# Kernel optimization log

Measured on AMD Instinct MI355X. Metric: run time of the kernel, lower is better.

Reference implementation:

```python
import jax, jax.numpy as jnp
import numpy as np

BS, SEQ, D, H, NK = 4, 256, 256, 8, 16


def _ln(x, g, b, eps=1e-5):
    m = x.mean(-1, keepdims=True)
    v = ((x - m) ** 2).mean(-1, keepdims=True)
    return (x - m) / jnp.sqrt(v + eps) * g + b


def _attention(q, k, v, mask, gammas, maxout):
    # q,k,v: [b,h,s,dk]; mask: [1,1,s,s] bool; gammas: [h,1,1]
    dk = q.shape[-1]
    scores = jnp.einsum('bhqd,bhkd->bhqk', q, k) / jnp.sqrt(jnp.asarray(dk, q.dtype))
    seqlen = scores.shape[-1]
    ar = jnp.arange(seqlen)
    pos = jnp.abs(ar[None, :] - ar[:, None]).astype(scores.dtype)[None, None]
    # distance-decay term (computed under no_grad in the original)
    s_ = jax.nn.softmax(jnp.where(mask, scores, -1e32), axis=-1)
    distcum = jnp.cumsum(s_, axis=-1)
    disttotal = jnp.sum(s_, axis=-1, keepdims=True)
    dist = jax.lax.stop_gradient(jnp.sqrt(jnp.clip((disttotal - distcum) * pos, 0.0, None)))
    g = -jnp.abs(gammas)[None]  # [1,h,1,1]
    effect = jnp.clip(jnp.exp(dist * g), 1e-5, 1e5)
    scores = scores * effect
    scores = jax.nn.softmax(jnp.where(mask, scores, -1e32), axis=-1)
    scores = jnp.where(mask, scores, 0.0)
    if maxout:
        scale = jnp.minimum(1.0 / (jnp.max(scores, axis=-1, keepdims=True) + 1e-8), 5.0)
        scores = scores * scale
    return jnp.einsum('bhqk,bhkd->bhqd', scores, v), scores


def _mha(xq, xk, xv, Wq, bq, Wk, bk, Wv, bv, Wo, bo, gammas, mask, maxout):
    bs, seq, d = xq.shape
    h = gammas.shape[0]
    dk = d // h
    def heads(x, W, b):
        return (x @ W + b).reshape(bs, seq, h, dk).transpose(0, 2, 1, 3)
    o, sc = _attention(heads(xq, Wq, bq), heads(xk, Wk, bk), heads(xv, Wv, bv), mask, gammas, maxout)
    o = o.transpose(0, 2, 1, 3).reshape(bs, seq, d)
    return o @ Wo + bo, sc


def _block(xq, xk, xv, Wq, bq, Wk, bk, Wv, bv, Wo, bo, gammas, lng, lnb, peek_cur):
    seq = xq.shape[1]
    mask = jnp.tril(jnp.ones((seq, seq), bool), 0 if peek_cur else -1)[None, None]
    out, sc = _mha(xq, xk, xv, Wq, bq, Wk, bk, Wv, bv, Wo, bo, gammas, mask, not peek_cur)
    return _ln(xq + out, lng, lnb), sc


def _dtransformer(q_emb, s_emb, know_params,
                  Wq1, bq1, Wv1, bv1, Wo1, bo1, gam1, lng1, lnb1,
                  Wq2, bq2, Wv2, bv2, Wo2, bo2, gam2, lng2, lnb2,
                  Wq3, bq3, Wv3, bv3, Wo3, bo3, gam3, lng3, lnb3,
                  Wq4, bq4, Wk4, bk4, Wv4, bv4, Wo4, bo4, gam4, lng4, lnb4):
    # n_blocks == 3 path; kq_same=True for blocks 1-3 (Wk := Wq)
    hq, _ = _block(q_emb, q_emb, q_emb, Wq1, bq1, Wq1, bq1, Wv1, bv1, Wo1, bo1, gam1, lng1, lnb1, True)
    hs, _ = _block(s_emb, s_emb, s_emb, Wq2, bq2, Wq2, bq2, Wv2, bv2, Wo2, bo2, gam2, lng2, lnb2, True)
    p, q_scores = _block(hq, hq, hs, Wq3, bq3, Wq3, bq3, Wv3, bv3, Wo3, bo3, gam3, lng3, lnb3, True)
    bs, seq, d = p.shape
    nk = know_params.shape[0]
    query = jnp.broadcast_to(know_params[None, :, None, :], (bs, nk, seq, d)).reshape(bs * nk, seq, d)
    hq_r = jnp.broadcast_to(hq[:, None], (bs, nk, seq, d)).reshape(bs * nk, seq, d)
    p_r = jnp.broadcast_to(p[:, None], (bs, nk, seq, d)).reshape(bs * nk, seq, d)
    z, k_sc = _block(query, hq_r, p_r, Wq4, bq4, Wk4, bk4, Wv4, bv4, Wo4, bo4, gam4, lng4, lnb4, False)
    z = z.reshape(bs, nk, seq, d).transpose(0, 2, 1, 3).reshape(bs, seq, nk * d)
    h = gam4.shape[0]
    k_scores = k_sc.reshape(bs, nk, h, seq, seq).transpose(0, 2, 3, 1, 4)
    return z, q_scores, k_scores


_PARAM_NAMES = []
for _b in ('1', '2', '3', '4'):
    _PARAM_NAMES += ['Wq' + _b, 'bq' + _b]
    if _b == '4':
        _PARAM_NAMES += ['Wk4', 'bk4']
    _PARAM_NAMES += ['Wv' + _b, 'bv' + _b, 'Wo' + _b, 'bo' + _b, 'gam' + _b, 'lng' + _b, 'lnb' + _b]


def setup_inputs() -> dict:
    key = jax.random.key(0)
    ks = jax.random.split(key, 64)
    inp = {}
    inp['q_emb'] = jax.random.normal(ks[0], (BS, SEQ, D), jnp.float32)
    inp['s_emb'] = jax.random.normal(ks[1], (BS, SEQ, D), jnp.float32)
    inp['lens'] = jax.random.randint(ks[2], (BS,), 1, SEQ)
    inp['know_params'] = jax.random.uniform(ks[3], (NK, D), jnp.float32, -1.0, 1.0)
    i = 4
    for name in _PARAM_NAMES:
        if name.startswith('W'):
            inp[name] = jax.random.normal(ks[i], (D, D), jnp.float32) * 0.02; i += 1
        elif name.startswith('b'):
            inp[name] = jnp.zeros((D,), jnp.float32)
        elif name.startswith('gam'):
            inp[name] = jax.random.normal(ks[i], (H, 1, 1), jnp.float32) * 0.3; i += 1
        elif name.startswith('lng'):
            inp[name] = jnp.ones((D,), jnp.float32)
        else:
            inp[name] = jnp.zeros((D,), jnp.float32)
    return inp


def reference(q_emb, s_emb, lens, know_params,
              Wq1, bq1, Wv1, bv1, Wo1, bo1, gam1, lng1, lnb1,
              Wq2, bq2, Wv2, bv2, Wo2, bo2, gam2, lng2, lnb2,
              Wq3, bq3, Wv3, bv3, Wo3, bo3, gam3, lng3, lnb3,
              Wq4, bq4, Wk4, bk4, Wv4, bv4, Wo4, bo4, gam4, lng4, lnb4):
    return _dtransformer(q_emb, s_emb, know_params,
                         Wq1, bq1, Wv1, bv1, Wo1, bo1, gam1, lng1, lnb1,
                         Wq2, bq2, Wv2, bv2, Wo2, bo2, gam2, lng2, lnb2,
                         Wq3, bq3, Wv3, bv3, Wo3, bo3, gam3, lng3, lnb3,
                         Wq4, bq4, Wk4, bk4, Wv4, bv4, Wo4, bo4, gam4, lng4, lnb4)
```

## Files before the change

kernel.cpp:

```cpp
#include <hip/hip_runtime.h>
#include <math.h>

#define SEQL 256
#define DM   256
#define NH   8
#define DKH  32
#define BSZ  4
#define NKN  16

__device__ __forceinline__ float wave_red_sum(float v) {
#pragma unroll
  for (int o = 32; o > 0; o >>= 1) v += __shfl_xor(v, o);
  return v;
}
__device__ __forceinline__ float wave_red_max(float v) {
#pragma unroll
  for (int o = 32; o > 0; o >>= 1) v = fmaxf(v, __shfl_xor(v, o));
  return v;
}
__device__ __forceinline__ float wave_incl_scan(float v) {
  const int lane = threadIdx.x & 63;
#pragma unroll
  for (int o = 1; o < 64; o <<= 1) {
    float u = __shfl_up(v, o);
    if (lane >= o) v += u;
  }
  return v;
}

struct GemmSet { const float* A; const float* W; const float* bias; float* C; int M; };
struct Gemm4 { GemmSet s[4]; };

__global__ __launch_bounds__(256) void dt_gemmN(Gemm4 args) {
  const GemmSet g = args.s[blockIdx.z];
  const int bm = blockIdx.x * 64, bn = blockIdx.y * 64;
  if (bm >= g.M) return;
  __shared__ float As[16][68];
  __shared__ float Bs[16][68];
  const int tid = threadIdx.x;
  const int tc = tid & 15, tr = tid >> 4;
  float acc[4][4] = {};
  for (int k0 = 0; k0 < DM; k0 += 16) {
    {
      const int m = tid >> 2, kq = tid & 3;
      int row = bm + m; row = row < g.M ? row : (g.M - 1);
      const float4 v = *reinterpret_cast<const float4*>(&g.A[(size_t)row * DM + k0 + kq * 4]);
      As[kq * 4 + 0][m] = v.x; As[kq * 4 + 1][m] = v.y;
      As[kq * 4 + 2][m] = v.z; As[kq * 4 + 3][m] = v.w;
    }
    {
      const int k = tid >> 4, nq = tid & 15;
      const float4 v = *reinterpret_cast<const float4*>(&g.W[(size_t)(k0 + k) * DM + bn + nq * 4]);
      *reinterpret_cast<float4*>(&Bs[k][nq * 4]) = v;
    }
    __syncthreads();
#pragma unroll
    for (int k = 0; k < 16; ++k) {
      float a[4], b[4];
#pragma unroll
      for (int i = 0; i < 4; ++i) a[i] = As[k][tr * 4 + i];
#pragma unroll
      for (int j = 0; j < 4; ++j) b[j] = Bs[k][tc * 4 + j];
#pragma unroll
      for (int i = 0; i < 4; ++i)
#pragma unroll
        for (int j = 0; j < 4; ++j) acc[i][j] = fmaf(a[i], b[j], acc[i][j]);
    }
    __syncthreads();
  }
#pragma unroll
  for (int i = 0; i < 4; ++i) {
    const int row = bm + tr * 4 + i;
    if (row >= g.M) continue;
    float4 o;
    o.x = acc[i][0] + g.bias[bn + tc * 4 + 0];
    o.y = acc[i][1] + g.bias[bn + tc * 4 + 1];
    o.z = acc[i][2] + g.bias[bn + tc * 4 + 2];
    o.w = acc[i][3] + g.bias[bn + tc * 4 + 3];
    *reinterpret_cast<float4*>(&g.C[(size_t)row * DM + bn + tc * 4]) = o;
  }
}

__global__ __launch_bounds__(256) void dt_scores_nt2(const float* __restrict__ Q0,
                                                     const float* __restrict__ Q1,
                                                     float* __restrict__ Sa,
                                                     float* __restrict__ Sb) {
  const int z = blockIdx.z;
  const int set = z >> 5, bh = z & 31;
  const float* Qp = set ? Q1 : Q0;
  float* S = set ? Sb : Sa;
  const int b = bh >> 3, h = bh & 7;
  const float* Q = Qp + (size_t)b * SEQL * DM + h * DKH;
  __shared__ float Qs[16][33], Ks[16][33];
  const int tid = threadIdx.x;
  const int tj = tid & 15, ti = tid >> 4;
  const int i0 = blockIdx.x * 16, j0 = blockIdx.y * 16;
  const int r = tid >> 5, c = tid & 31;
  Qs[r][c]     = Q[(size_t)(i0 + r) * DM + c];
  Qs[r + 8][c] = Q[(size_t)(i0 + 8 + r) * DM + c];
  Ks[r][c]     = Q[(size_t)(j0 + r) * DM + c];
  Ks[r + 8][c] = Q[(size_t)(j0 + 8 + r) * DM + c];
  __syncthreads();
  float acc = 0.f;
#pragma unroll
  for (int k = 0; k < DKH; ++k) acc = fmaf(Qs[ti][k], Ks[tj][k], acc);
  S[((size_t)bh * SEQL + i0 + ti) * SEQL + j0 + tj] = acc * 0.17677669529663687f;
}

__global__ __launch_bounds__(256) void dt_scores4(const float* __restrict__ Q4h,
                                                  const float* __restrict__ Kp,
                                                  float* __restrict__ S0) {
  const int idx = blockIdx.x * 256 + threadIdx.x;
  const int j = idx & 255;
  const int h = (idx >> 8) & 7;
  const int nk = (idx >> 11) & 15;
  const int b = idx >> 15;
  const float* q = Q4h + nk * DM + h * DKH;
  const float* k = Kp + ((size_t)(b * SEQL + j)) * DM + h * DKH;
  float acc = 0.f;
#pragma unroll
  for (int c = 0; c < DKH; ++c) acc = fmaf(q[c], k[c], acc);
  S0[idx] = acc * 0.17677669529663687f;
}

__global__ __launch_bounds__(256) void dt_prep4(const float* __restrict__ S0,
                                                float* __restrict__ Pfx) {
  const int wid = threadIdx.x >> 6, lane = threadIdx.x & 63;
  const int row = blockIdx.x * 4 + wid;
  const float4 s4 = *reinterpret_cast<const float4*>(S0 + (size_t)row * SEQL + lane * 4);
  float s[4] = {s4.x, s4.y, s4.z, s4.w};
  float mx = fmaxf(fmaxf(s[0], s[1]), fmaxf(s[2], s[3]));
  mx = wave_red_max(mx);
  float e[4], t = 0.f;
#pragma unroll
  for (int q = 0; q < 4; ++q) { e[q] = __expf(s[q] - mx); t += e[q]; }
  const float incl = wave_incl_scan(t);
  float run = incl - t;
  float4 o;
  run += e[0]; o.x = run;
  run += e[1]; o.y = run;
  run += e[2]; o.z = run;
  run += e[3]; o.w = run;
  *reinterpret_cast<float4*>(Pfx + (size_t)row * SEQL + lane * 4) = o;
}

__global__ __launch_bounds__(256) void dt_softmax13w2(const float* __restrict__ Sa,
                                                      const float* __restrict__ Sb,
                                                      float* __restrict__ Pa,
                                                      float* __restrict__ Pb,
                                                      const float* __restrict__ g0,
                                                      const float* __restrict__ g1) {
  const int wid = threadIdx.x >> 6, lane = threadIdx.x & 63;
  const int grow = blockIdx.x * 4 + wid;
  const int set = grow >> 13;
  const int row = grow & 8191;
  const float* S = set ? Sb : Sa;
  float* P = set ? Pb : Pa;
  const float* gam = set ? g1 : g0;
  const int i = row & 255, h = (row >> 8) & 7;
  const float g = -fabsf(gam[h]);
  const int jb = lane * 4;
  const float4 s4 = *reinterpret_cast<const float4*>(S + (size_t)row * SEQL + jb);
  float s[4] = {s4.x, s4.y, s4.z, s4.w};
  float mx = -1e30f;
#pragma unroll
  for (int q = 0; q < 4; ++q) if (jb + q <= i) mx = fmaxf(mx, s[q]);
  mx = wave_red_max(mx);
  float e[4], t = 0.f;
#pragma unroll
  for (int q = 0; q < 4; ++q) { e[q] = (jb + q <= i) ? __expf(s[q] - mx) : 0.f; t += e[q]; }
  const float incl = wave_incl_scan(t);
  const float total = __shfl(incl, 63);
  const float inv = 1.f / total;
  float run = incl - t;
  float p2[4], t2 = 0.f;
#pragma unroll
  for (int q = 0; q < 4; ++q) {
    run += e[q];
    const float cum = run * inv;
    float dd = (1.f - cum) * (float)(i - jb - q);
    dd = dd > 0.f ? dd : 0.f;
    float eff = __expf(g * sqrtf(dd));
    eff = fmaxf(eff, 1e-5f);
    const float y = s[q] * eff;
    p2[q] = (jb + q <= i) ? __expf(y) : 0.f;
    t2 += p2[q];
  }
  const float sum2 = wave_red_sum(t2);
  const float inv2 = 1.f / sum2;
  float4 o = {p2[0] * inv2, p2[1] * inv2, p2[2] * inv2, p2[3] * inv2};
  *reinterpret_cast<float4*>(P + (size_t)row * SEQL + jb) = o;
}

__global__ __launch_bounds__(256) void dt_sm_pv4(const float* __restrict__ S0,
                                                 const float* __restrict__ Pfx,
                                                 const float* __restrict__ Vp,
                                                 const float* __restrict__ gam,
                                                 float* __restrict__ KS,
                                                 float* __restrict__ O) {
  __shared__ float Vs[256][32];
  __shared__ float Pl[32][260];
  __shared__ float Pfl[256];
  const int z = blockIdx.x;
  const int h = z & 7, b = z >> 7;
  const int nk = (z >> 3) & 15, bnk = z >> 3;
  const int tid = threadIdx.x, lane = tid & 63, w = tid >> 6;
  const float* Vbase = Vp + (size_t)b * SEQL * DM + h * DKH;
  {
    const int j = tid >> 3, c4 = (tid & 7) * 4;
    for (int jj = 0; jj < 256; jj += 32) {
      const float4 v = *reinterpret_cast<const float4*>(Vbase + (size_t)(jj + j) * DM + c4);
      *reinterpret_cast<float4*>(&Vs[jj + j][c4]) = v;
    }
  }
  if (tid < 64) {
    const float4 p = *reinterpret_cast<const float4*>(Pfx + (size_t)z * SEQL + tid * 4);
    *reinterpret_cast<float4*>(&Pfl[tid * 4]) = p;
  }
  const float4 s4 = *reinterpret_cast<const float4*>(S0 + (size_t)z * SEQL + lane * 4);
  const float4 p4 = *reinterpret_cast<const float4*>(Pfx + (size_t)z * SEQL + lane * 4);
  const float s[4] = {s4.x, s4.y, s4.z, s4.w};
  const float pj[4] = {p4.x, p4.y, p4.z, p4.w};
  const float g = -fabsf(gam[h]);
  const int jb = lane * 4;
  __syncthreads();

  for (int chunk = 0; chunk < 8; ++chunk) {
    const int i0 = chunk * 32;
#pragma unroll
    for (int r = 0; r < 8; ++r) {
      const int il = w * 8 + r;
      const int i = i0 + il;
      float pv[4];
      if (i == 0) {
        pv[0] = pv[1] = pv[2] = pv[3] = 0.f;
      } else {
        const float rinv = 1.f / Pfl[i - 1];
        float t = 0.f, m = 0.f;
#pragma unroll
        for (int q = 0; q < 4; ++q) {
          const float cum = pj[q] * rinv;
          float dd = (1.f - cum) * (float)(i - jb - q);
          dd = dd > 0.f ? dd : 0.f;
          float eff = __expf(g * sqrtf(dd));
          eff = fmaxf(eff, 1e-5f);
          const float y = s[q] * eff;
          pv[q] = (jb + q < i) ? __expf(y) : 0.f;
          t += pv[q];
          m = fmaxf(m, pv[q]);
        }
#pragma unroll
        for (int o = 32; o > 0; o >>= 1) {
          t += __shfl_xor(t, o);
          m = fmaxf(m, __shfl_xor(m, o));
        }
        const float inv2 = 1.f / t;
        const float scale = fminf(1.f / (m * inv2 + 1e-8f), 5.f);
        const float f = inv2 * scale;
        pv[0] *= f; pv[1] *= f; pv[2] *= f; pv[3] *= f;
      }
      const float4 o4 = {pv[0], pv[1], pv[2], pv[3]};
      *reinterpret_cast<float4*>(KS + ((((size_t)(b * NH + h)) * SEQL + i) * NKN + nk) * SEQL + jb) = o4;
      *reinterpret_cast<float4*>(&Pl[il][jb]) = o4;
    }
    __syncthreads();
    const int il = tid >> 3, cg = tid & 7;
    float ax = 0.f, ay = 0.f, az = 0.f, aw = 0.f;
#pragma unroll 8
    for (int j4 = 0; j4 < 64; ++j4) {
      const float4 pp = *reinterpret_cast<const float4*>(&Pl[il][j4 * 4]);
      const float4 v0 = *reinterpret_cast<const float4*>(&Vs[j4 * 4 + 0][cg * 4]);
      const float4 v1 = *reinterpret_cast<const float4*>(&Vs[j4 * 4 + 1][cg * 4]);
      const float4 v2 = *reinterpret_cast<const float4*>(&Vs[j4 * 4 + 2][cg * 4]);
      const float4 v3 = *reinterpret_cast<const float4*>(&Vs[j4 * 4 + 3][cg * 4]);
      ax = fmaf(pp.x, v0.x, ax); ax = fmaf(pp.y, v1.x, ax); ax = fmaf(pp.z, v2.x, ax); ax = fmaf(pp.w, v3.x, ax);
      ay = fmaf(pp.x, v0.y, ay); ay = fmaf(pp.y, v1.y, ay); ay = fmaf(pp.z, v2.y, ay); ay = fmaf(pp.w, v3.y, ay);
      az = fmaf(pp.x, v0.z, az); az = fmaf(pp.y, v1.z, az); az = fmaf(pp.z, v2.z, az); az = fmaf(pp.w, v3.z, az);
      aw = fmaf(pp.x, v0.w, aw); aw = fmaf(pp.y, v1.w, aw); aw = fmaf(pp.z, v2.w, aw); aw = fmaf(pp.w, v3.w, aw);
    }
    const float4 oo = {ax, ay, az, aw};
    *reinterpret_cast<float4*>(O + ((size_t)(bnk * SEQL + i0 + il)) * DM + h * DKH + cg * 4) = oo;
    __syncthreads();
  }
}

__global__ __launch_bounds__(256) void dt_pv13_2(const float* __restrict__ Pa,
                                                 const float* __restrict__ Pb,
                                                 const float* __restrict__ V0,
                                                 const float* __restrict__ V1,
                                                 float* __restrict__ Oa,
                                                 float* __restrict__ Ob) {
  __shared__ float Ps[32][33];
  __shared__ float Vs[32][33];
  const int z = blockIdx.y;
  const int set = z >> 5, bh = z & 31;
  const float* P = set ? Pb : Pa;
  const float* Vp = set ? V1 : V0;
  float* O = set ? Ob : Oa;
  const int b = bh >> 3, h = bh & 7;
  const int i0 = blockIdx.x * 32;
  const int tid = threadIdx.x;
  const int c = tid & 31, ir = tid >> 5;
  float acc[4] = {0.f, 0.f, 0.f, 0.f};
  const float* Prow = P + ((size_t)bh * SEQL + i0) * SEQL;
  const float* Vbase = Vp + (size_t)b * SEQL * DM + h * DKH;
  for (int j0 = 0; j0 < SEQL; j0 += 32) {
#pragma unroll
    for (int k = 0; k < 4; ++k) {
      Ps[ir + k * 8][c] = Prow[(size_t)(ir + k * 8) * SEQL + j0 + c];
      Vs[ir + k * 8][c] = Vbase[(size_t)(j0 + ir + k * 8) * DM + c];
    }
    __syncthreads();
#pragma unroll
    for (int jj = 0; jj < 32; ++jj) {
      const float v = Vs[jj][c];
#pragma unroll
      for (int k = 0; k < 4; ++k) acc[k] = fmaf(Ps[ir + k * 8][jj], v, acc[k]);
    }
    __syncthreads();
  }
#pragma unroll
  for (int k = 0; k < 4; ++k)
    O[((size_t)(b * SEQL + i0 + ir + k * 8)) * DM + h * DKH + c] = acc[k];
}

__global__ __launch_bounds__(256) void dt_ln_res2(const float* __restrict__ X0,
                                                  const float* __restrict__ X1,
                                                  const float* __restrict__ Y0,
                                                  const float* __restrict__ Y1,
                                                  const float* __restrict__ G0,
                                                  const float* __restrict__ G1,
                                                  const float* __restrict__ B0,
                                                  const float* __restrict__ B1,
                                                  float* __restrict__ Z0,
                                                  float* __restrict__ Z1) {
  const int wid = threadIdx.x >> 6, lane = threadIdx.x & 63;
  const int grow = blockIdx.x * 4 + wid;
  const int set = grow >> 10;
  const int row = grow & 1023;
  const float* X = set ? X1 : X0;
  const float* Y = set ? Y1 : Y0;
  const float* g = set ? G1 : G0;
  const float* bb = set ? B1 : B0;
  float* Z = set ? Z1 : Z0;
  const int jb = lane * 4;
  const float4 x4 = *reinterpret_cast<const float4*>(X + (size_t)row * DM + jb);
  const float4 y4 = *reinterpret_cast<const float4*>(Y + (size_t)row * DM + jb);
  float x[4] = {x4.x + y4.x, x4.y + y4.y, x4.z + y4.z, x4.w + y4.w};
  const float mean = wave_red_sum(x[0] + x[1] + x[2] + x[3]) * (1.f / 256.f);
  float vs = 0.f;
#pragma unroll
  for (int q = 0; q < 4; ++q) { const float d = x[q] - mean; vs += d * d; }
  const float var = wave_red_sum(vs) * (1.f / 256.f);
  const float rstd = 1.f / sqrtf(var + 1e-5f);
  const float4 g4 = *reinterpret_cast<const float4*>(g + jb);
  const float4 b4 = *reinterpret_cast<const float4*>(bb + jb);
  float4 o;
  o.x = (x[0] - mean) * rstd * g4.x + b4.x;
  o.y = (x[1] - mean) * rstd * g4.y + b4.y;
  o.z = (x[2] - mean) * rstd * g4.z + b4.z;
  o.w = (x[3] - mean) * rstd * g4.w + b4.w;
  *reinterpret_cast<float4*>(Z + (size_t)row * DM + jb) = o;
}

__global__ __launch_bounds__(256) void dt_ln4w(const float* __restrict__ know,
                                               const float* __restrict__ Y,
                                               const float* __restrict__ g,
                                               const float* __restrict__ bb,
                                               float* __restrict__ Z) {
  const int wid = threadIdx.x >> 6, lane = threadIdx.x & 63;
  const int row = blockIdx.x * 4 + wid;
  const int i = row & 255;
  const int nk = (row >> 8) & 15;
  const int b = row >> 12;
  const int jb = lane * 4;
  const float4 k4 = *reinterpret_cast<const float4*>(know + (size_t)nk * DM + jb);
  const float4 y4 = *reinterpret_cast<const float4*>(Y + (size_t)row * DM + jb);
  float x[4] = {k4.x + y4.x, k4.y + y4.y, k4.z + y4.z, k4.w + y4.w};
  const float mean = wave_red_sum(x[0] + x[1] + x[2] + x[3]) * (1.f / 256.f);
  float vs = 0.f;
#pragma unroll
  for (int q = 0; q < 4; ++q) { const float d = x[q] - mean; vs += d * d; }
  const float var = wave_red_sum(vs) * (1.f / 256.f);
  const float rstd = 1.f / sqrtf(var + 1e-5f);
  const float4 g4 = *reinterpret_cast<const float4*>(g + jb);
  const float4 b4 = *reinterpret_cast<const float4*>(bb + jb);
  float4 o;
  o.x = (x[0] - mean) * rstd * g4.x + b4.x;
  o.y = (x[1] - mean) * rstd * g4.y + b4.y;
  o.z = (x[2] - mean) * rstd * g4.z + b4.z;
  o.w = (x[3] - mean) * rstd * g4.w + b4.w;
  *reinterpret_cast<float4*>(Z + ((size_t)(b * SEQL + i)) * (NKN * DM) + (size_t)nk * DM + jb) = o;
}

extern "C" void kernel_launch(void* const* d_in, const int* in_sizes, int n_in,
                              void* d_out, int out_size, void* d_ws, size_t ws_size,
                              hipStream_t stream) {
  (void)in_sizes; (void)n_in; (void)out_size; (void)ws_size;
  const float* q_emb = (const float*)d_in[0];
  const float* s_emb = (const float*)d_in[1];
  const float* know  = (const float*)d_in[3];
  const float* Wq1 = (const float*)d_in[4],  *bq1 = (const float*)d_in[5];
  const float* Wv1 = (const float*)d_in[6],  *bv1 = (const float*)d_in[7];
  const float* Wo1 = (const float*)d_in[8],  *bo1 = (const float*)d_in[9];
  const float* gam1 = (const float*)d_in[10], *lng1 = (const float*)d_in[11], *lnb1 = (const float*)d_in[12];
  const float* Wq2 = (const float*)d_in[13], *bq2 = (const float*)d_in[14];
  const float* Wv2 = (const float*)d_in[15], *bv2 = (const float*)d_in[16];
  const float* Wo2 = (const float*)d_in[17], *bo2 = (const float*)d_in[18];
  const float* gam2 = (const float*)d_in[19], *lng2 = (const float*)d_in[20], *lnb2 = (const float*)d_in[21];
  const float* Wq3 = (const float*)d_in[22], *bq3 = (const float*)d_in[23];
  const float* Wv3 = (const float*)d_in[24], *bv3 = (const float*)d_in[25];
  const float* Wo3 = (const float*)d_in[26], *bo3 = (const float*)d_in[27];
  const float* gam3 = (const float*)d_in[28], *lng3 = (const float*)d_in[29], *lnb3 = (const float*)d_in[30];
  const float* Wq4 = (const float*)d_in[31], *bq4 = (const float*)d_in[32];
  const float* Wk4 = (const float*)d_in[33], *bk4 = (const float*)d_in[34];
  const float* Wv4 = (const float*)d_in[35], *bv4 = (const float*)d_in[36];
  const float* Wo4 = (const float*)d_in[37], *bo4 = (const float*)d_in[38];
  const float* gam4 = (const float*)d_in[39], *lng4 = (const float*)d_in[40], *lnb4 = (const float*)d_in[41];

  float* ws = (float*)d_ws;
  const size_t U = 262144;
  float* Qp0 = ws + 0 * U;
  float* Qp1 = ws + 1 * U;
  float* Vp0 = ws + 2 * U;
  float* Vp1 = ws + 3 * U;
  float* Sa  = ws + 4 * U;
  float* Sb  = ws + 12 * U;
  float* O0  = ws + 20 * U;
  float* O1  = ws + 21 * U;
  float* OW0 = ws + 22 * U;
  float* OW1 = ws + 23 * U;
  float* hq  = ws + 24 * U;
  float* hs  = ws + 25 * U;
  float* pbf = ws + 26 * U;
  float* Q4h = ws + 27 * U;
  float* S0s = Q4h + 4096;
  float* OW4 = Sa;
  float* Pfx = O0;

  float* zout = (float*)d_out;
  float* qsc  = zout + 4194304;
  float* ksc  = qsc + 2097152;
  float* O4   = zout;

  const dim3 thr(256);

  {
    Gemm4 a = {{{q_emb, Wq1, bq1, Qp0, 1024}, {q_emb, Wv1, bv1, Vp0, 1024},
                {s_emb, Wq2, bq2, Qp1, 1024}, {s_emb, Wv2, bv2, Vp1, 1024}}};
    dt_gemmN<<<dim3(16, 4, 4), thr, 0, stream>>>(a);
  }
  dt_scores_nt2<<<dim3(16, 16, 64), thr, 0, stream>>>(Qp0, Qp1, Sa, Sb);
  dt_softmax13w2<<<dim3(4096), thr, 0, stream>>>(Sa, Sb, Sa, Sb, gam1, gam2);
  dt_pv13_2<<<dim3(8, 64), thr, 0, stream>>>(Sa, Sb, Vp0, Vp1, O0, O1);
  {
    Gemm4 a = {{{O0, Wo1, bo1, OW0, 1024}, {O1, Wo2, bo2, OW1, 1024},
                {O0, Wo1, bo1, OW0, 1024}, {O1, Wo2, bo2, OW1, 1024}}};
    dt_gemmN<<<dim3(16, 4, 2), thr, 0, stream>>>(a);
  }
  dt_ln_res2<<<dim3(512), thr, 0, stream>>>(q_emb, s_emb, OW0, OW1, lng1, lng2, lnb1, lnb2, hq, hs);

  {
    Gemm4 a = {{{hq, Wq3, bq3, Qp0, 1024}, {hs, Wv3, bv3, Vp0, 1024},
                {hq, Wq3, bq3, Qp0, 1024}, {hs, Wv3, bv3, Vp0, 1024}}};
    dt_gemmN<<<dim3(16, 4, 2), thr, 0, stream>>>(a);
  }
  dt_scores_nt2<<<dim3(16, 16, 32), thr, 0, stream>>>(Qp0, Qp0, Sa, Sa);
  dt_softmax13w2<<<dim3(2048), thr, 0, stream>>>(Sa, Sa, qsc, qsc, gam3, gam3);
  dt_pv13_2<<<dim3(8, 32), thr, 0, stream>>>(qsc, qsc, Vp0, Vp0, O0, O0);
  {
    Gemm4 a = {{{O0, Wo3, bo3, OW0, 1024}, {O0, Wo3, bo3, OW0, 1024},
                {O0, Wo3, bo3, OW0, 1024}, {O0, Wo3, bo3, OW0, 1024}}};
    dt_gemmN<<<dim3(16, 4, 1), thr, 0, stream>>>(a);
  }
  dt_ln_res2<<<dim3(256), thr, 0, stream>>>(hq, hq, OW0, OW0, lng3, lng3, lnb3, lnb3, pbf, pbf);

  {
    Gemm4 a = {{{hq, Wk4, bk4, Qp0, 1024}, {pbf, Wv4, bv4, Vp0, 1024},
                {know, Wq4, bq4, Q4h, 16}, {know, Wq4, bq4, Q4h, 16}}};
    dt_gemmN<<<dim3(16, 4, 3), thr, 0, stream>>>(a);
  }
  dt_scores4<<<dim3(512), thr, 0, stream>>>(Q4h, Qp0, S0s);
  dt_prep4<<<dim3(128), thr, 0, stream>>>(S0s, Pfx);
  dt_sm_pv4<<<dim3(512), thr, 0, stream>>>(S0s, Pfx, Vp0, gam4, ksc, O4);
  {
    Gemm4 a = {{{O4, Wo4, bo4, OW4, 16384}, {O4, Wo4, bo4, OW4, 16384},
                {O4, Wo4, bo4, OW4, 16384}, {O4, Wo4, bo4, OW4, 16384}}};
    dt_gemmN<<<dim3(256, 4, 1), thr, 0, stream>>>(a);
  }
  dt_ln4w<<<dim3(4096), thr, 0, stream>>>(know, OW4, lng4, lnb4, zout);
}
```

Before: 530.0 us.

## Register-block P·V products with 4x4 tiles and split-k shuffle reduction

Rewrites the P·V inner loops in dt_sm_pv4 and dt_pv13_2 so each thread computes a 4-row by 4-column register tile over a quarter of the key dimension, then combines partial sums across lanes with xor shuffles. This raises FMA-per-LDS-load reuse, since each P float4 and V float4 is used four times. dt_pv13_2 also drops its 32-wide j loop with per-tile barriers in favour of loading the whole V slice and P tile into shared memory at once with float4 loads. In exchange the code gains shuffle reductions, masked stores, larger shared memory (lower occupancy in pv13_2) and different LDS bank patterns, handled by padding Pl to 268.

```diff
diff --git a/kernel.cpp b/kernel.cpp
--- a/kernel.cpp
+++ b/kernel.cpp
@@ -199,7 +199,7 @@
                                                  float* __restrict__ KS,
                                                  float* __restrict__ O) {
   __shared__ float Vs[256][32];
-  __shared__ float Pl[32][260];
+  __shared__ float Pl[32][268];
   __shared__ float Pfl[256];
   const int z = blockIdx.x;
   const int h = z & 7, b = z >> 7;
@@ -223,6 +223,7 @@
   const float pj[4] = {p4.x, p4.y, p4.z, p4.w};
   const float g = -fabsf(gam[h]);
   const int jb = lane * 4;
+  const int r0 = tid >> 5, cg = tid & 7, jq = (tid >> 3) & 3;
   __syncthreads();
 
   for (int chunk = 0; chunk < 8; ++chunk) {
@@ -264,22 +265,40 @@
       *reinterpret_cast<float4*>(&Pl[il][jb]) = o4;
     }
     __syncthreads();
-    const int il = tid >> 3, cg = tid & 7;
-    float ax = 0.f, ay = 0.f, az = 0.f, aw = 0.f;
-#pragma unroll 8
-    for (int j4 = 0; j4 < 64; ++j4) {
-      const float4 pp = *reinterpret_cast<const float4*>(&Pl[il][j4 * 4]);
-      const float4 v0 = *reinterpret_cast<const float4*>(&Vs[j4 * 4 + 0][cg * 4]);
-      const float4 v1 = *reinterpret_cast<const float4*>(&Vs[j4 * 4 + 1][cg * 4]);
-      const float4 v2 = *reinterpret_cast<const float4*>(&Vs[j4 * 4 + 2][cg * 4]);
-      const float4 v3 = *reinterpret_cast<const float4*>(&Vs[j4 * 4 + 3][cg * 4]);
-      ax = fmaf(pp.x, v0.x, ax); ax = fmaf(pp.y, v1.x, ax); ax = fmaf(pp.z, v2.x, ax); ax = fmaf(pp.w, v3.x, ax);
-      ay = fmaf(pp.x, v0.y, ay); ay = fmaf(pp.y, v1.y, ay); ay = fmaf(pp.z, v2.y, ay); ay = fmaf(pp.w, v3.y, ay);
-      az = fmaf(pp.x, v0.z, az); az = fmaf(pp.y, v1.z, az); az = fmaf(pp.z, v2.z, az); az = fmaf(pp.w, v3.z, az);
-      aw = fmaf(pp.x, v0.w, aw); aw = fmaf(pp.y, v1.w, aw); aw = fmaf(pp.z, v2.w, aw); aw = fmaf(pp.w, v3.w, aw);
-    }
-    const float4 oo = {ax, ay, az, aw};
-    *reinterpret_cast<float4*>(O + ((size_t)(bnk * SEQL + i0 + il)) * DM + h * DKH + cg * 4) = oo;
+    float4 acc[4] = {{0.f,0.f,0.f,0.f},{0.f,0.f,0.f,0.f},{0.f,0.f,0.f,0.f},{0.f,0.f,0.f,0.f}};
+#pragma unroll 4
+    for (int t4 = 0; t4 < 16; ++t4) {
+      const int jb2 = t4 * 16 + jq * 4;
+      float pr[4][4];
+#pragma unroll
+      for (int r = 0; r < 4; ++r) {
+        const float4 p = *reinterpret_cast<const float4*>(&Pl[r0 * 4 + r][jb2]);
+        pr[r][0] = p.x; pr[r][1] = p.y; pr[r][2] = p.z; pr[r][3] = p.w;
+      }
+#pragma unroll
+      for (int k = 0; k < 4; ++k) {
+        const float4 v = *reinterpret_cast<const float4*>(&Vs[jb2 + k][cg * 4]);
+#pragma unroll
+        for (int r = 0; r < 4; ++r) {
+          acc[r].x = fmaf(pr[r][k], v.x, acc[r].x);
+          acc[r].y = fmaf(pr[r][k], v.y, acc[r].y);
+          acc[r].z = fmaf(pr[r][k], v.z, acc[r].z);
+          acc[r].w = fmaf(pr[r][k], v.w, acc[r].w);
+        }
+      }
+    }
+#pragma unroll
+    for (int r = 0; r < 4; ++r) {
+      acc[r].x += __shfl_xor(acc[r].x, 8);  acc[r].x += __shfl_xor(acc[r].x, 16);
+      acc[r].y += __shfl_xor(acc[r].y, 8);  acc[r].y += __shfl_xor(acc[r].y, 16);
+      acc[r].z += __shfl_xor(acc[r].z, 8);  acc[r].z += __shfl_xor(acc[r].z, 16);
+      acc[r].w += __shfl_xor(acc[r].w, 8);  acc[r].w += __shfl_xor(acc[r].w, 16);
+    }
+    if ((tid & 24) == 0) {
+#pragma unroll
+      for (int r = 0; r < 4; ++r)
+        *reinterpret_cast<float4*>(O + ((size_t)(bnk * SEQL + i0 + r0 * 4 + r)) * DM + h * DKH + cg * 4) = acc[r];
+    }
     __syncthreads();
   }
 }
@@ -290,8 +309,8 @@
                                                  const float* __restrict__ V1,
                                                  float* __restrict__ Oa,
                                                  float* __restrict__ Ob) {
-  __shared__ float Ps[32][33];
-  __shared__ float Vs[32][33];
+  __shared__ float Vs[256][32];
+  __shared__ float Pl[32][268];
   const int z = blockIdx.y;
   const int set = z >> 5, bh = z & 31;
   const float* P = set ? Pb : Pa;
@@ -300,28 +319,54 @@
   const int b = bh >> 3, h = bh & 7;
   const int i0 = blockIdx.x * 32;
   const int tid = threadIdx.x;
-  const int c = tid & 31, ir = tid >> 5;
-  float acc[4] = {0.f, 0.f, 0.f, 0.f};
   const float* Prow = P + ((size_t)bh * SEQL + i0) * SEQL;
   const float* Vbase = Vp + (size_t)b * SEQL * DM + h * DKH;
-  for (int j0 = 0; j0 < SEQL; j0 += 32) {
+#pragma unroll
+  for (int t = 0; t < 8; ++t) {
+    const int idx = t * 256 + tid;
+    const int j = idx >> 3, c4 = (idx & 7) * 4;
+    *reinterpret_cast<float4*>(&Vs[j][c4]) =
+        *reinterpret_cast<const float4*>(Vbase + (size_t)j * DM + c4);
+    const int prw = idx >> 6, pc4 = (idx & 63) * 4;
+    *reinterpret_cast<float4*>(&Pl[prw][pc4]) =
+        *reinterpret_cast<const float4*>(Prow + (size_t)prw * SEQL + pc4);
+  }
+  __syncthreads();
+  const int r0 = tid >> 5, cg = tid & 7, jq = (tid >> 3) & 3;
+  float4 acc[4] = {{0.f,0.f,0.f,0.f},{0.f,0.f,0.f,0.f},{0.f,0.f,0.f,0.f},{0.f,0.f,0.f,0.f}};
+#pragma unroll 4
+  for (int t4 = 0; t4 < 16; ++t4) {
+    const int jb2 = t4 * 16 + jq * 4;
+    float pr[4][4];
+#pragma unroll
+    for (int r = 0; r < 4; ++r) {
+      const float4 p = *reinterpret_cast<const float4*>(&Pl[r0 * 4 + r][jb2]);
+      pr[r][0] = p.x; pr[r][1] = p.y; pr[r][2] = p.z; pr[r][3] = p.w;
+    }
 #pragma unroll
     for (int k = 0; k < 4; ++k) {
-      Ps[ir + k * 8][c] = Prow[(size_t)(ir + k * 8) * SEQL + j0 + c];
-      Vs[ir + k * 8][c] = Vbase[(size_t)(j0 + ir + k * 8) * DM + c];
-    }
-    __syncthreads();
-#pragma unroll
-    for (int jj = 0; jj < 32; ++jj) {
-      const float v = Vs[jj][c];
-#pragma unroll
-      for (int k = 0; k < 4; ++k) acc[k] = fmaf(Ps[ir + k * 8][jj], v, acc[k]);
-    }
-    __syncthreads();
-  }
-#pragma unroll
-  for (int k = 0; k < 4; ++k)
-    O[((size_t)(b * SEQL + i0 + ir + k * 8)) * DM + h * DKH + c] = acc[k];
+      const float4 v = *reinterpret_cast<const float4*>(&Vs[jb2 + k][cg * 4]);
+#pragma unroll
+      for (int r = 0; r < 4; ++r) {
+        acc[r].x = fmaf(pr[r][k], v.x, acc[r].x);
+        acc[r].y = fmaf(pr[r][k], v.y, acc[r].y);
+        acc[r].z = fmaf(pr[r][k], v.z, acc[r].z);
+        acc[r].w = fmaf(pr[r][k], v.w, acc[r].w);
+      }
+    }
+  }
+#pragma unroll
+  for (int r = 0; r < 4; ++r) {
+    acc[r].x += __shfl_xor(acc[r].x, 8);  acc[r].x += __shfl_xor(acc[r].x, 16);
+    acc[r].y += __shfl_xor(acc[r].y, 8);  acc[r].y += __shfl_xor(acc[r].y, 16);
+    acc[r].z += __shfl_xor(acc[r].z, 8);  acc[r].z += __shfl_xor(acc[r].z, 16);
+    acc[r].w += __shfl_xor(acc[r].w, 8);  acc[r].w += __shfl_xor(acc[r].w, 16);
+  }
+  if ((tid & 24) == 0) {
+#pragma unroll
+    for (int r = 0; r < 4; ++r)
+      *reinterpret_cast<float4*>(O + ((size_t)(b * SEQL + i0 + r0 * 4 + r)) * DM + h * DKH + cg * 4) = acc[r];
+  }
 }
 
 __global__ __launch_bounds__(256) void dt_ln_res2(const float* __restrict__ X0,
```

Result: faster. 516.1 us (-2.6%).
